# Performance work log

Measured on AMD Instinct MI355X. Metric: run time of the kernel, lower is better.

## Reference

```python
import jax, jax.numpy as jnp
import numpy as np

N_USERS = 40000
N_ITEMS = 20000
NNZ = 1_000_000
D = 64
N_LAYERS = 3
EPS = 1e-8
PRUNING = 0.0  # forward default: pruning=0.0 -> get_sim_adj branch, threshold is a no-op


def setup_inputs() -> dict:
    key = jax.random.key(0)
    k1, k2, k3 = jax.random.split(key, 3)
    # unique-ish sorted edge codes -> coalesced COO order (sorted by (u, i))
    codes = jnp.sort(jax.random.randint(k3, (NNZ,), 0, N_USERS * N_ITEMS, dtype=jnp.int32))
    u_idx = codes // N_ITEMS
    i_idx = codes % N_ITEMS
    # xavier_uniform bound = sqrt(6/(fan_in+fan_out))
    b_u = float(np.sqrt(6.0 / (N_ITEMS + D)))
    b_i = float(np.sqrt(6.0 / (N_USERS + D)))
    user_linear = jax.random.uniform(k1, (N_ITEMS, D), jnp.float32, -b_u, b_u)
    item_linear = jax.random.uniform(k2, (N_USERS, D), jnp.float32, -b_i, b_i)
    return {"user_linear": user_linear, "item_linear": item_linear,
            "u_idx": u_idx, "i_idx": i_idx}


def reference(user_linear, item_linear, u_idx, i_idx):
    seg = jax.ops.segment_sum
    N = N_USERS + N_ITEMS
    # get_all_user_embedding: inter @ user_linear  -> [n_users, D]
    user_emb = seg(user_linear[i_idx], u_idx, num_segments=N_USERS)
    # get_all_item_embedding: inter.T @ item_linear -> [n_items, D]
    item_emb = seg(item_linear[u_idx], i_idx, num_segments=N_ITEMS)

    # sp_cos_sim: per-edge cosine similarity (chunked loop in torch == one vectorized gather)
    u_n = user_emb / jnp.maximum(jnp.linalg.norm(user_emb, axis=1, keepdims=True), EPS)
    i_n = item_emb / jnp.maximum(jnp.linalg.norm(item_emb, axis=1, keepdims=True), EPS)
    sims = jnp.sum(u_n[u_idx] * i_n[i_idx], axis=1)  # [nnz]
    # torch builds the sim sparse tensor with requires_grad=False -> detached
    sims = jax.lax.stop_gradient(sims)

    # inter2adj: values = [sims sorted by (u,i); sims sorted by (i,u)]
    sim_value = (sims + 1.0) * 0.5
    sim_value = jnp.where(sim_value < PRUNING, 0.0, sim_value) if PRUNING > 0 else sim_value
    perm = jnp.argsort(i_idx.astype(jnp.int32) * N_USERS + u_idx)  # (i,u) coalesce order
    rows = jnp.concatenate([u_idx, i_idx[perm] + N_USERS])          # [2*nnz]
    cols = jnp.concatenate([i_idx + N_USERS, u_idx[perm]])
    vals = jnp.concatenate([sim_value, sim_value[perm]])

    # row-normalize: D^-1 * A  (get_sim_adj)
    diags = seg(vals, rows, num_segments=N) + 1e-7
    vals = vals * (1.0 / diags)[rows]

    # LightGCN-style propagation
    all_emb = jnp.concatenate([user_emb, item_emb], axis=0)  # [N, D]
    embs = [all_emb]
    for _ in range(N_LAYERS):
        all_emb = seg(all_emb[cols] * vals[:, None], rows, num_segments=N)
        embs.append(all_emb)
    out = jnp.mean(jnp.stack(embs, axis=1), axis=1)  # [N, D]
    return out[:N_USERS], out[N_USERS:]
```

## Files before the change

kernel.cpp:

```cpp
#include <hip/hip_runtime.h>
#include <hip/hip_fp16.h>

#define N_USERS 40000
#define N_ITEMS 20000
#define N_TOTAL (N_USERS + N_ITEMS)
#define D 64
#define G_BKT ((N_ITEMS + 63) >> 6)
#define PAD 16

union H8 { uint4 u; __half h[8]; };

#define ZA (N_ITEMS * D / 8)
#define ZB (N_USERS * D / 8)
#define ZC (N_USERS + 1)
#define ZD ((G_BKT + 1) * PAD)
#define ZTOT (ZA + ZB + ZC + ZD)

__global__ void setup_kernel(const float* __restrict__ ul, const float* __restrict__ il,
                             const int* __restrict__ u_idx,
                             __half* __restrict__ ulH, __half* __restrict__ ilH,
                             int* __restrict__ pu, int* __restrict__ bcnt, int nnz) {
    int t = blockIdx.x * blockDim.x + threadIdx.x;
    if (t < ZA) {
        const float4* s = (const float4*)(ul + (size_t)t * 8);
        float4 a = s[0], b = s[1];
        H8 o;
        o.h[0] = __float2half(a.x); o.h[1] = __float2half(a.y);
        o.h[2] = __float2half(a.z); o.h[3] = __float2half(a.w);
        o.h[4] = __float2half(b.x); o.h[5] = __float2half(b.y);
        o.h[6] = __float2half(b.z); o.h[7] = __float2half(b.w);
        ((uint4*)ulH)[t] = o.u;
    } else if (t < ZA + ZB) {
        int q = t - ZA;
        const float4* s = (const float4*)(il + (size_t)q * 8);
        float4 a = s[0], b = s[1];
        H8 o;
        o.h[0] = __float2half(a.x); o.h[1] = __float2half(a.y);
        o.h[2] = __float2half(a.z); o.h[3] = __float2half(a.w);
        o.h[4] = __float2half(b.x); o.h[5] = __float2half(b.y);
        o.h[6] = __float2half(b.z); o.h[7] = __float2half(b.w);
        ((uint4*)ilH)[q] = o.u;
    } else if (t < ZA + ZB + ZC) {
        int u = t - (ZA + ZB);
        int lo = 0, hi = nnz;
        while (lo < hi) { int mid = (lo + hi) >> 1; if (u_idx[mid] < u) lo = mid + 1; else hi = mid; }
        pu[u] = lo;
    } else if (t < ZTOT) {
        bcnt[t - (ZA + ZB + ZC)] = 0;
    }
}


__global__ void bcount_kernel(const int* __restrict__ i_idx, int* __restrict__ bcnt, int nnz) {
    __shared__ int lc[G_BKT];
    for (int t = threadIdx.x; t < G_BKT; t += blockDim.x) lc[t] = 0;
    __syncthreads();
    int stride = gridDim.x * blockDim.x;
    for (int e = blockIdx.x * blockDim.x + threadIdx.x; e < nnz; e += stride)
        atomicAdd(&lc[__builtin_nontemporal_load(i_idx + e) >> 6], 1);
    __syncthreads();
    for (int t = threadIdx.x; t < G_BKT; t += blockDim.x)
        if (lc[t]) atomicAdd(bcnt + t * PAD, lc[t]);
}

__global__ void bscan_kernel(const int* __restrict__ bcnt, int* __restrict__ bbase,
                             int* __restrict__ bcur, int* __restrict__ pi, int nnz) {
    if (threadIdx.x == 0 && blockIdx.x == 0) {
        int run = 0;
        for (int g = 0; g < G_BKT; ++g) {
            bbase[g * PAD] = run;
            bcur[g * PAD] = run;
            run += bcnt[g * PAD];
        }
        bbase[G_BKT * PAD] = run;
        pi[N_ITEMS] = run;
    }
}

__global__ void p1_kernel(const int* __restrict__ i_idx, const int* __restrict__ u_idx,
                          int* __restrict__ bcur, int2* __restrict__ tmp, int nnz) {
    const int E = 8;
    __shared__ int lc[G_BKT];
    __shared__ int gb[G_BKT];
    for (int t = threadIdx.x; t < G_BKT; t += blockDim.x) lc[t] = 0;
    __syncthreads();
    int base_e = blockIdx.x * blockDim.x * E;
    int myb[E], myr[E]; int2 myv[E];
    #pragma unroll
    for (int j = 0; j < E; ++j) {
        int e = base_e + j * blockDim.x + threadIdx.x;
        myb[j] = -1;
        if (e < nnz) {
            int i = __builtin_nontemporal_load(i_idx + e);
            int u = __builtin_nontemporal_load(u_idx + e);
            int b = i >> 6;
            myb[j] = b;
            myr[j] = atomicAdd(&lc[b], 1);
            myv[j] = make_int2(e, (i << 16) | u);
        }
    }
    __syncthreads();
    for (int t = threadIdx.x; t < G_BKT; t += blockDim.x)
        gb[t] = lc[t] ? atomicAdd(bcur + t * PAD, lc[t]) : 0;
    __syncthreads();
    #pragma unroll
    for (int j = 0; j < E; ++j)
        if (myb[j] >= 0) tmp[gb[myb[j]] + myr[j]] = myv[j];
}

__global__ void p2_kernel(const int2* __restrict__ tmp, const int* __restrict__ bbase,
                          int* __restrict__ pi, int* __restrict__ eids, int* __restrict__ col2) {
    __shared__ int hist[64];
    __shared__ int cur[64];
    int g = blockIdx.x;
    int t = threadIdx.x;
    if (t < 64) { hist[t] = 0; cur[t] = 0; }
    __syncthreads();
    int base = bbase[g * PAD], end = bbase[(g + 1) * PAD];
    int lo_item = g << 6;
    for (int k = base + t; k < end; k += blockDim.x)
        atomicAdd(&hist[(tmp[k].y >> 16) & 63], 1);
    __syncthreads();
    if (t == 0) {
        int run = base;
        for (int x = 0; x < 64; ++x) {
            int c = hist[x];
            hist[x] = run;
            if (lo_item + x < N_ITEMS) pi[lo_item + x] = run;
            run += c;
        }
    }
    __syncthreads();
    for (int k = base + t; k < end; k += blockDim.x) {
        int2 v = tmp[k];
        int li = (v.y >> 16) & 63;
        int pos = atomicAdd(&cur[li], 1);
        int dst = hist[li] + pos;
        eids[dst] = v.x;
        col2[dst] = v.y & 0xFFFF;
    }
}

__global__ void emb_kernel(const __half* __restrict__ ulH, const __half* __restrict__ ilH,
                           const int* __restrict__ i_idx, const int* __restrict__ col2,
                           const int* __restrict__ pu, const int* __restrict__ pi,
                           __half* __restrict__ embH, float* __restrict__ invn) {
    int tid = blockIdx.x * blockDim.x + threadIdx.x;
    int wave = tid >> 6, lane = threadIdx.x & 63;
    int g = lane >> 3, c = lane & 7;
    int row = wave * 8 + g;
    if (row >= N_TOTAL) return;
    float s[8];
    #pragma unroll
    for (int j = 0; j < 8; ++j) s[j] = 0.f;
    const __half* tbl; const int* cols; int b, e;
    if (row < N_USERS) { tbl = ulH; cols = i_idx; b = pu[row]; e = pu[row + 1]; }
    else { int i = row - N_USERS; tbl = ilH; cols = col2; b = pi[i]; e = pi[i + 1]; }
    int k = b;
    for (; k + 3 < e; k += 4) {
        int i0 = cols[k], i1 = cols[k + 1], i2 = cols[k + 2], i3 = cols[k + 3];
        H8 r0, r1, r2, r3;
        r0.u = ((const uint4*)(tbl + (size_t)i0 * D))[c];
        r1.u = ((const uint4*)(tbl + (size_t)i1 * D))[c];
        r2.u = ((const uint4*)(tbl + (size_t)i2 * D))[c];
        r3.u = ((const uint4*)(tbl + (size_t)i3 * D))[c];
        #pragma unroll
        for (int q = 0; q < 8; ++q)
            s[q] += (__half2float(r0.h[q]) + __half2float(r1.h[q]))
                  + (__half2float(r2.h[q]) + __half2float(r3.h[q]));
    }
    for (; k < e; ++k) {
        H8 r0;
        r0.u = ((const uint4*)(tbl + (size_t)cols[k] * D))[c];
        #pragma unroll
        for (int q = 0; q < 8; ++q) s[q] += __half2float(r0.h[q]);
    }
    float nsq = 0.f;
    #pragma unroll
    for (int q = 0; q < 8; ++q) nsq += s[q] * s[q];
    #pragma unroll
    for (int m = 1; m < 8; m <<= 1) nsq += __shfl_xor(nsq, m, 64);
    H8 o;
    #pragma unroll
    for (int q = 0; q < 8; ++q) o.h[q] = __float2half(s[q]);
    ((uint4*)(embH + (size_t)row * D))[c] = o.u;
    if (c == 0) invn[row] = 1.f / fmaxf(sqrtf(nsq), 1e-8f);
}

__global__ void fsp1u_kernel(const __half* __restrict__ embA, const float* __restrict__ invn,
                             const int* __restrict__ i_idx, const int* __restrict__ pu,
                             float* __restrict__ sims, float* __restrict__ diag,
                             __half* __restrict__ embB) {
    int tid = blockIdx.x * blockDim.x + threadIdx.x;
    int wave = tid >> 6, lane = threadIdx.x & 63;
    int g = lane >> 3, c = lane & 7;
    int u = wave * 8 + g;
    if (u >= N_USERS) return;
    float invu = invn[u];
    H8 ur; ur.u = ((const uint4*)(embA + (size_t)u * D))[c];
    float un[8];
    #pragma unroll
    for (int q = 0; q < 8; ++q) un[q] = __half2float(ur.h[q]) * invu;
    float s[8];
    #pragma unroll
    for (int q = 0; q < 8; ++q) s[q] = 0.f;
    float dsum = 0.f;
    int b = pu[u], e = pu[u + 1];
    int k = b;
    for (; k + 3 < e; k += 4) {
        int i0 = i_idx[k], i1 = i_idx[k + 1], i2 = i_idx[k + 2], i3 = i_idx[k + 3];
        H8 r0, r1, r2, r3;
        r0.u = ((const uint4*)(embA + (size_t)(N_USERS + i0) * D))[c];
        r1.u = ((const uint4*)(embA + (size_t)(N_USERS + i1) * D))[c];
        r2.u = ((const uint4*)(embA + (size_t)(N_USERS + i2) * D))[c];
        r3.u = ((const uint4*)(embA + (size_t)(N_USERS + i3) * D))[c];
        float iv0 = invn[N_USERS + i0], iv1 = invn[N_USERS + i1];
        float iv2 = invn[N_USERS + i2], iv3 = invn[N_USERS + i3];
        float d0 = 0.f, d1 = 0.f, d2 = 0.f, d3 = 0.f;
        #pragma unroll
        for (int q = 0; q < 8; ++q) {
            d0 += un[q] * __half2float(r0.h[q]);
            d1 += un[q] * __half2float(r1.h[q]);
            d2 += un[q] * __half2float(r2.h[q]);
            d3 += un[q] * __half2float(r3.h[q]);
        }
        #pragma unroll
        for (int m = 1; m < 8; m <<= 1) {
            d0 += __shfl_xor(d0, m, 64); d1 += __shfl_xor(d1, m, 64);
            d2 += __shfl_xor(d2, m, 64); d3 += __shfl_xor(d3, m, 64);
        }
        float sv0 = (d0 * iv0 + 1.f) * 0.5f;
        float sv1 = (d1 * iv1 + 1.f) * 0.5f;
        float sv2 = (d2 * iv2 + 1.f) * 0.5f;
        float sv3 = (d3 * iv3 + 1.f) * 0.5f;
        if (c == 0) { sims[k] = sv0; sims[k + 1] = sv1; sims[k + 2] = sv2; sims[k + 3] = sv3; }
        dsum += (sv0 + sv1) + (sv2 + sv3);
        #pragma unroll
        for (int q = 0; q < 8; ++q)
            s[q] += (sv0 * __half2float(r0.h[q]) + sv1 * __half2float(r1.h[q]))
                  + (sv2 * __half2float(r2.h[q]) + sv3 * __half2float(r3.h[q]));
    }
    for (; k < e; ++k) {
        int i0 = i_idx[k];
        H8 r0;
        r0.u = ((const uint4*)(embA + (size_t)(N_USERS + i0) * D))[c];
        float iv0 = invn[N_USERS + i0];
        float d0 = 0.f;
        #pragma unroll
        for (int q = 0; q < 8; ++q) d0 += un[q] * __half2float(r0.h[q]);
        #pragma unroll
        for (int m = 1; m < 8; m <<= 1) d0 += __shfl_xor(d0, m, 64);
        float sv0 = (d0 * iv0 + 1.f) * 0.5f;
        if (c == 0) sims[k] = sv0;
        dsum += sv0;
        #pragma unroll
        for (int q = 0; q < 8; ++q) s[q] += sv0 * __half2float(r0.h[q]);
    }
    if (c == 0) diag[u] = dsum;
    float invd = 1.f / (dsum + 1e-7f);
    H8 o;
    #pragma unroll
    for (int q = 0; q < 8; ++q) o.h[q] = __float2half(s[q] * invd);
    ((uint4*)(embB + (size_t)u * D))[c] = o.u;
}

__global__ void p1i_kernel(const __half* __restrict__ embA, const float* __restrict__ sims,
                           const int* __restrict__ eids, const int* __restrict__ col2,
                           const int* __restrict__ pi, float* __restrict__ w2,
                           float* __restrict__ diag, __half* __restrict__ embB) {
    int tid = blockIdx.x * blockDim.x + threadIdx.x;
    int wave = tid >> 6, lane = threadIdx.x & 63;
    int g = lane >> 3, c = lane & 7;
    int i = wave * 8 + g;
    if (i >= N_ITEMS) return;
    float s[8];
    #pragma unroll
    for (int q = 0; q < 8; ++q) s[q] = 0.f;
    float dsum = 0.f;
    int b = pi[i], e = pi[i + 1];
    int k = b;
    for (; k + 3 < e; k += 4) {
        int e0 = eids[k], e1 = eids[k + 1], e2 = eids[k + 2], e3 = eids[k + 3];
        int u0 = col2[k], u1 = col2[k + 1], u2 = col2[k + 2], u3 = col2[k + 3];
        float w0 = sims[e0], w1 = sims[e1], w2v = sims[e2], w3v = sims[e3];
        H8 r0, r1, r2, r3;
        r0.u = ((const uint4*)(embA + (size_t)u0 * D))[c];
        r1.u = ((const uint4*)(embA + (size_t)u1 * D))[c];
        r2.u = ((const uint4*)(embA + (size_t)u2 * D))[c];
        r3.u = ((const uint4*)(embA + (size_t)u3 * D))[c];
        if (c == 0) { w2[k] = w0; w2[k + 1] = w1; w2[k + 2] = w2v; w2[k + 3] = w3v; }
        dsum += (w0 + w1) + (w2v + w3v);
        #pragma unroll
        for (int q = 0; q < 8; ++q)
            s[q] += (w0 * __half2float(r0.h[q]) + w1 * __half2float(r1.h[q]))
                  + (w2v * __half2float(r2.h[q]) + w3v * __half2float(r3.h[q]));
    }
    for (; k < e; ++k) {
        float w0 = sims[eids[k]];
        H8 r0;
        r0.u = ((const uint4*)(embA + (size_t)col2[k] * D))[c];
        if (c == 0) w2[k] = w0;
        dsum += w0;
        #pragma unroll
        for (int q = 0; q < 8; ++q) s[q] += w0 * __half2float(r0.h[q]);
    }
    if (c == 0) diag[N_USERS + i] = dsum;
    float invd = 1.f / (dsum + 1e-7f);
    H8 o;
    #pragma unroll
    for (int q = 0; q < 8; ++q) o.h[q] = __float2half(s[q] * invd);
    ((uint4*)(embB + (size_t)(N_USERS + i) * D))[c] = o.u;
}

template <bool FINAL>
__global__ void prop_kernel(const __half* __restrict__ curH, __half* __restrict__ nextH,
                            const float* __restrict__ sims, const float* __restrict__ w2,
                            const float* __restrict__ diag,
                            const int* __restrict__ i_idx, const int* __restrict__ col2,
                            const int* __restrict__ pu, const int* __restrict__ pi,
                            const __half* __restrict__ e0, const __half* __restrict__ e1,
                            const __half* __restrict__ e2, float* __restrict__ out) {
    int tid = blockIdx.x * blockDim.x + threadIdx.x;
    int wave = tid >> 6, lane = threadIdx.x & 63;
    int g = lane >> 3, c = lane & 7;
    int row = wave * 8 + g;
    if (row >= N_TOTAL) return;
    float s[8];
    #pragma unroll
    for (int j = 0; j < 8; ++j) s[j] = 0.f;
    const int* cols; const float* ws; int b, e, colOff;
    if (row < N_USERS) { b = pu[row]; e = pu[row + 1]; cols = i_idx; ws = sims; colOff = N_USERS; }
    else { int i = row - N_USERS; b = pi[i]; e = pi[i + 1]; cols = col2; ws = w2; colOff = 0; }
    int k = b;
    for (; k + 3 < e; k += 4) {
        int i0 = cols[k] + colOff, i1 = cols[k + 1] + colOff,
            i2 = cols[k + 2] + colOff, i3 = cols[k + 3] + colOff;
        float w0 = ws[k], w1 = ws[k + 1], w2v = ws[k + 2], w3v = ws[k + 3];
        H8 r0, r1, r2, r3;
        r0.u = ((const uint4*)(curH + (size_t)i0 * D))[c];
        r1.u = ((const uint4*)(curH + (size_t)i1 * D))[c];
        r2.u = ((const uint4*)(curH + (size_t)i2 * D))[c];
        r3.u = ((const uint4*)(curH + (size_t)i3 * D))[c];
        #pragma unroll
        for (int q = 0; q < 8; ++q)
            s[q] += (w0 * __half2float(r0.h[q]) + w1 * __half2float(r1.h[q]))
                  + (w2v * __half2float(r2.h[q]) + w3v * __half2float(r3.h[q]));
    }
    for (; k < e; ++k) {
        float w0 = ws[k];
        H8 r0;
        r0.u = ((const uint4*)(curH + (size_t)(cols[k] + colOff) * D))[c];
        #pragma unroll
        for (int q = 0; q < 8; ++q) s[q] += w0 * __half2float(r0.h[q]);
    }
    float invd = 1.f / (diag[row] + 1e-7f);
    float v[8];
    #pragma unroll
    for (int q = 0; q < 8; ++q) v[q] = s[q] * invd;
    if (FINAL) {
        H8 r0, r1, r2;
        r0.u = ((const uint4*)(e0 + (size_t)row * D))[c];
        r1.u = ((const uint4*)(e1 + (size_t)row * D))[c];
        r2.u = ((const uint4*)(e2 + (size_t)row * D))[c];
        float o[8];
        #pragma unroll
        for (int q = 0; q < 8; ++q)
            o[q] = (v[q] + __half2float(r0.h[q]) + __half2float(r1.h[q]) + __half2float(r2.h[q])) * 0.25f;
        float4* op = (float4*)(out + (size_t)row * D);
        op[c * 2]     = make_float4(o[0], o[1], o[2], o[3]);
        op[c * 2 + 1] = make_float4(o[4], o[5], o[6], o[7]);
    } else {
        H8 o;
        #pragma unroll
        for (int q = 0; q < 8; ++q) o.h[q] = __float2half(v[q]);
        ((uint4*)(nextH + (size_t)row * D))[c] = o.u;
    }
}


extern "C" void kernel_launch(void* const* d_in, const int* in_sizes, int n_in,
                              void* d_out, int out_size, void* d_ws, size_t ws_size,
                              hipStream_t stream) {
    const float* user_linear = (const float*)d_in[0];
    const float* item_linear = (const float*)d_in[1];
    const int* u_idx = (const int*)d_in[2];
    const int* i_idx = (const int*)d_in[3];
    const int nnz = in_sizes[2];

    char* p = (char*)d_ws;
    auto carve = [&](size_t bytes) { void* r = (void*)p; p += (bytes + 255) & ~(size_t)255; return r; };
    __half* embA = (__half*)carve((size_t)N_TOTAL * D * 2);
    __half* embB = (__half*)carve((size_t)N_TOTAL * D * 2);
    __half* embC = (__half*)carve((size_t)N_TOTAL * D * 2);
    __half* ulH  = (__half*)carve((size_t)N_ITEMS * D * 2);
    __half* ilH  = (__half*)carve((size_t)N_USERS * D * 2);
    float* sims = (float*)carve((size_t)nnz * 4);
    float* w2   = (float*)carve((size_t)nnz * 4);
    float* diag = (float*)carve((size_t)N_TOTAL * 4);
    float* invn = (float*)carve((size_t)N_TOTAL * 4);
    int* pu   = (int*)carve((size_t)(N_USERS + 1) * 4);
    int* pi   = (int*)carve((size_t)(N_ITEMS + 1) * 4);
    int* eids = (int*)carve((size_t)nnz * 4);
    int* col2 = (int*)carve((size_t)nnz * 4);
    int* bcnt  = (int*)carve((size_t)(G_BKT + 1) * PAD * 4);
    int* bbase = (int*)carve((size_t)(G_BKT + 1) * PAD * 4);
    int* bcur  = (int*)carve((size_t)(G_BKT + 1) * PAD * 4);

    int2* tmp = (int2*)embA;

    float* out = (float*)d_out;

    const int B = 256;

    setup_kernel<<<(ZTOT + B - 1) / B, B, 0, stream>>>(user_linear, item_linear, u_idx,
                                                       ulH, ilH, pu, bcnt, nnz);
    bcount_kernel<<<256, B, 0, stream>>>(i_idx, bcnt, nnz);
    bscan_kernel<<<1, 64, 0, stream>>>(bcnt, bbase, bcur, pi, nnz);
    p1_kernel<<<(nnz + B * 8 - 1) / (B * 8), B, 0, stream>>>(i_idx, u_idx, bcur, tmp, nnz);
    p2_kernel<<<G_BKT, B, 0, stream>>>(tmp, bbase, pi, eids, col2);

    int rowThreads = ((N_TOTAL + 7) / 8) * 64;
    emb_kernel<<<(rowThreads + B - 1) / B, B, 0, stream>>>(ulH, ilH, i_idx, col2,
                                                           pu, pi, embA, invn);

    int uThreads = ((N_USERS + 7) / 8) * 64;
    fsp1u_kernel<<<(uThreads + B - 1) / B, B, 0, stream>>>(embA, invn, i_idx, pu,
                                                           sims, diag, embB);
    int iThreads = ((N_ITEMS + 7) / 8) * 64;
    p1i_kernel<<<(iThreads + B - 1) / B, B, 0, stream>>>(embA, sims, eids, col2, pi,
                                                         w2, diag, embB);

    prop_kernel<false><<<(rowThreads + B - 1) / B, B, 0, stream>>>(embB, embC, sims, w2, diag,
                                                                   i_idx, col2, pu, pi,
                                                                   nullptr, nullptr, nullptr, nullptr);
    prop_kernel<true><<<(rowThreads + B - 1) / B, B, 0, stream>>>(embC, nullptr, sims, w2, diag,
                                                                  i_idx, col2, pu, pi,
                                                                  embA, embB, embC, out);
}
```

Before: 232.8 us.

## Use nontemporal loads/stores for streamed data and remap row blocks across XCDs

Marks streamed index arrays, edge weights and per-row output writes as nontemporal so they do not evict the gathered embedding tables from cache. Also adds a block-to-row mapping for the full-grid kernels that interleaves blocks mod 8, so each XCD works on a contiguous range of user or item rows and the gathered rows stay local to that XCD's L2. The gain depends on hardware cache behaviour. The hardcoded grid mapping ties the code to the fixed problem sizes.

Result: slower. 336.6 us (+44.6%).

```diff
diff --git a/kernel.cpp b/kernel.cpp
--- a/kernel.cpp
+++ b/kernel.cpp
@@ -9,6 +9,40 @@
 #define PAD 16
 
 union H8 { uint4 u; __half h[8]; };
+
+typedef unsigned int u32x4 __attribute__((ext_vector_type(4)));
+typedef float f32x4 __attribute__((ext_vector_type(4)));
+typedef int i32x2 __attribute__((ext_vector_type(2)));
+
+#define NTL(x) __builtin_nontemporal_load(&(x))
+
+__device__ __forceinline__ void nt_store_u4(uint4 v, void* p) {
+    u32x4 t = { v.x, v.y, v.z, v.w };
+    __builtin_nontemporal_store(t, (u32x4*)p);
+}
+__device__ __forceinline__ void nt_store_f4(float4 v, void* p) {
+    f32x4 t = { v.x, v.y, v.z, v.w };
+    __builtin_nontemporal_store(t, (f32x4*)p);
+}
+__device__ __forceinline__ int2 nt_load_i2(const void* p) {
+    i32x2 t = __builtin_nontemporal_load((const i32x2*)p);
+    return make_int2(t.x, t.y);
+}
+
+__device__ __forceinline__ int map_row(int bid, int wib, int g) {
+    int x = bid & 7, s = bid >> 3;
+    if (x < 5) {
+        int ub = x * 250 + s;
+        if (ub >= 1250) return -1;
+        return ub * 32 + wib * 8 + g;
+    } else {
+        int si = x - 5;
+        int cnt = (si == 2) ? 207 : 209;
+        if (s >= cnt) return -1;
+        return N_USERS + (si * 209 + s) * 32 + wib * 8 + g;
+    }
+}
+#define GRID_FULL 2000
 
 #define ZA (N_ITEMS * D / 8)
 #define ZB (N_USERS * D / 8)
@@ -119,7 +153,7 @@
     int base = bbase[g * PAD], end = bbase[(g + 1) * PAD];
     int lo_item = g << 6;
     for (int k = base + t; k < end; k += blockDim.x)
-        atomicAdd(&hist[(tmp[k].y >> 16) & 63], 1);
+        atomicAdd(&hist[(nt_load_i2(&tmp[k]).y >> 16) & 63], 1);
     __syncthreads();
     if (t == 0) {
         int run = base;
@@ -132,7 +166,7 @@
     }
     __syncthreads();
     for (int k = base + t; k < end; k += blockDim.x) {
-        int2 v = tmp[k];
+        int2 v = nt_load_i2(&tmp[k]);
         int li = (v.y >> 16) & 63;
         int pos = atomicAdd(&cur[li], 1);
         int dst = hist[li] + pos;
@@ -145,11 +179,10 @@
                            const int* __restrict__ i_idx, const int* __restrict__ col2,
                            const int* __restrict__ pu, const int* __restrict__ pi,
                            __half* __restrict__ embH, float* __restrict__ invn) {
-    int tid = blockIdx.x * blockDim.x + threadIdx.x;
-    int wave = tid >> 6, lane = threadIdx.x & 63;
+    int wib = threadIdx.x >> 6, lane = threadIdx.x & 63;
     int g = lane >> 3, c = lane & 7;
-    int row = wave * 8 + g;
-    if (row >= N_TOTAL) return;
+    int row = map_row(blockIdx.x, wib, g);
+    if (row < 0) return;
     float s[8];
     #pragma unroll
     for (int j = 0; j < 8; ++j) s[j] = 0.f;
@@ -158,7 +191,7 @@
     else { int i = row - N_USERS; tbl = ilH; cols = col2; b = pi[i]; e = pi[i + 1]; }
     int k = b;
     for (; k + 3 < e; k += 4) {
-        int i0 = cols[k], i1 = cols[k + 1], i2 = cols[k + 2], i3 = cols[k + 3];
+        int i0 = NTL(cols[k]), i1 = NTL(cols[k + 1]), i2 = NTL(cols[k + 2]), i3 = NTL(cols[k + 3]);
         H8 r0, r1, r2, r3;
         r0.u = ((const uint4*)(tbl + (size_t)i0 * D))[c];
         r1.u = ((const uint4*)(tbl + (size_t)i1 * D))[c];
@@ -171,7 +204,7 @@
     }
     for (; k < e; ++k) {
         H8 r0;
-        r0.u = ((const uint4*)(tbl + (size_t)cols[k] * D))[c];
+        r0.u = ((const uint4*)(tbl + (size_t)NTL(cols[k]) * D))[c];
         #pragma unroll
         for (int q = 0; q < 8; ++q) s[q] += __half2float(r0.h[q]);
     }
@@ -183,7 +216,7 @@
     H8 o;
     #pragma unroll
     for (int q = 0; q < 8; ++q) o.h[q] = __float2half(s[q]);
-    ((uint4*)(embH + (size_t)row * D))[c] = o.u;
+    nt_store_u4(o.u, (uint4*)(embH + (size_t)row * D) + c);
     if (c == 0) invn[row] = 1.f / fmaxf(sqrtf(nsq), 1e-8f);
 }
 
@@ -208,7 +241,7 @@
     int b = pu[u], e = pu[u + 1];
     int k = b;
     for (; k + 3 < e; k += 4) {
-        int i0 = i_idx[k], i1 = i_idx[k + 1], i2 = i_idx[k + 2], i3 = i_idx[k + 3];
+        int i0 = NTL(i_idx[k]), i1 = NTL(i_idx[k + 1]), i2 = NTL(i_idx[k + 2]), i3 = NTL(i_idx[k + 3]);
         H8 r0, r1, r2, r3;
         r0.u = ((const uint4*)(embA + (size_t)(N_USERS + i0) * D))[c];
         r1.u = ((const uint4*)(embA + (size_t)(N_USERS + i1) * D))[c];
@@ -233,7 +266,12 @@
         float sv1 = (d1 * iv1 + 1.f) * 0.5f;
         float sv2 = (d2 * iv2 + 1.f) * 0.5f;
         float sv3 = (d3 * iv3 + 1.f) * 0.5f;
-        if (c == 0) { sims[k] = sv0; sims[k + 1] = sv1; sims[k + 2] = sv2; sims[k + 3] = sv3; }
+        if (c == 0) {
+            __builtin_nontemporal_store(sv0, sims + k);
+            __builtin_nontemporal_store(sv1, sims + k + 1);
+            __builtin_nontemporal_store(sv2, sims + k + 2);
+            __builtin_nontemporal_store(sv3, sims + k + 3);
+        }
         dsum += (sv0 + sv1) + (sv2 + sv3);
         #pragma unroll
         for (int q = 0; q < 8; ++q)
@@ -241,7 +279,7 @@
                   + (sv2 * __half2float(r2.h[q]) + sv3 * __half2float(r3.h[q]));
     }
     for (; k < e; ++k) {
-        int i0 = i_idx[k];
+        int i0 = NTL(i_idx[k]);
         H8 r0;
         r0.u = ((const uint4*)(embA + (size_t)(N_USERS + i0) * D))[c];
         float iv0 = invn[N_USERS + i0];
@@ -251,7 +289,7 @@
         #pragma unroll
         for (int m = 1; m < 8; m <<= 1) d0 += __shfl_xor(d0, m, 64);
         float sv0 = (d0 * iv0 + 1.f) * 0.5f;
-        if (c == 0) sims[k] = sv0;
+        if (c == 0) __builtin_nontemporal_store(sv0, sims + k);
         dsum += sv0;
         #pragma unroll
         for (int q = 0; q < 8; ++q) s[q] += sv0 * __half2float(r0.h[q]);
@@ -261,7 +299,7 @@
     H8 o;
     #pragma unroll
     for (int q = 0; q < 8; ++q) o.h[q] = __float2half(s[q] * invd);
-    ((uint4*)(embB + (size_t)u * D))[c] = o.u;
+    nt_store_u4(o.u, (uint4*)(embB + (size_t)u * D) + c);
 }
 
 __global__ void p1i_kernel(const __half* __restrict__ embA, const float* __restrict__ sims,
@@ -280,15 +318,20 @@
     int b = pi[i], e = pi[i + 1];
     int k = b;
     for (; k + 3 < e; k += 4) {
-        int e0 = eids[k], e1 = eids[k + 1], e2 = eids[k + 2], e3 = eids[k + 3];
-        int u0 = col2[k], u1 = col2[k + 1], u2 = col2[k + 2], u3 = col2[k + 3];
+        int e0 = NTL(eids[k]), e1 = NTL(eids[k + 1]), e2 = NTL(eids[k + 2]), e3 = NTL(eids[k + 3]);
+        int u0 = NTL(col2[k]), u1 = NTL(col2[k + 1]), u2 = NTL(col2[k + 2]), u3 = NTL(col2[k + 3]);
         float w0 = sims[e0], w1 = sims[e1], w2v = sims[e2], w3v = sims[e3];
         H8 r0, r1, r2, r3;
         r0.u = ((const uint4*)(embA + (size_t)u0 * D))[c];
         r1.u = ((const uint4*)(embA + (size_t)u1 * D))[c];
         r2.u = ((const uint4*)(embA + (size_t)u2 * D))[c];
         r3.u = ((const uint4*)(embA + (size_t)u3 * D))[c];
-        if (c == 0) { w2[k] = w0; w2[k + 1] = w1; w2[k + 2] = w2v; w2[k + 3] = w3v; }
+        if (c == 0) {
+            __builtin_nontemporal_store(w0, w2 + k);
+            __builtin_nontemporal_store(w1, w2 + k + 1);
+            __builtin_nontemporal_store(w2v, w2 + k + 2);
+            __builtin_nontemporal_store(w3v, w2 + k + 3);
+        }
         dsum += (w0 + w1) + (w2v + w3v);
         #pragma unroll
         for (int q = 0; q < 8; ++q)
@@ -296,10 +339,10 @@
                   + (w2v * __half2float(r2.h[q]) + w3v * __half2float(r3.h[q]));
     }
     for (; k < e; ++k) {
-        float w0 = sims[eids[k]];
+        float w0 = sims[NTL(eids[k])];
         H8 r0;
-        r0.u = ((const uint4*)(embA + (size_t)col2[k] * D))[c];
-        if (c == 0) w2[k] = w0;
+        r0.u = ((const uint4*)(embA + (size_t)NTL(col2[k]) * D))[c];
+        if (c == 0) __builtin_nontemporal_store(w0, w2 + k);
         dsum += w0;
         #pragma unroll
         for (int q = 0; q < 8; ++q) s[q] += w0 * __half2float(r0.h[q]);
@@ -309,7 +352,7 @@
     H8 o;
     #pragma unroll
     for (int q = 0; q < 8; ++q) o.h[q] = __float2half(s[q] * invd);
-    ((uint4*)(embB + (size_t)(N_USERS + i) * D))[c] = o.u;
+    nt_store_u4(o.u, (uint4*)(embB + (size_t)(N_USERS + i) * D) + c);
 }
 
 template <bool FINAL>
@@ -320,11 +363,10 @@
                             const int* __restrict__ pu, const int* __restrict__ pi,
                             const __half* __restrict__ e0, const __half* __restrict__ e1,
                             const __half* __restrict__ e2, float* __restrict__ out) {
-    int tid = blockIdx.x * blockDim.x + threadIdx.x;
-    int wave = tid >> 6, lane = threadIdx.x & 63;
+    int wib = threadIdx.x >> 6, lane = threadIdx.x & 63;
     int g = lane >> 3, c = lane & 7;
-    int row = wave * 8 + g;
-    if (row >= N_TOTAL) return;
+    int row = map_row(blockIdx.x, wib, g);
+    if (row < 0) return;
     float s[8];
     #pragma unroll
     for (int j = 0; j < 8; ++j) s[j] = 0.f;
@@ -333,9 +375,9 @@
     else { int i = row - N_USERS; b = pi[i]; e = pi[i + 1]; cols = col2; ws = w2; colOff = 0; }
     int k = b;
     for (; k + 3 < e; k += 4) {
-        int i0 = cols[k] + colOff, i1 = cols[k + 1] + colOff,
-            i2 = cols[k + 2] + colOff, i3 = cols[k + 3] + colOff;
-        float w0 = ws[k], w1 = ws[k + 1], w2v = ws[k + 2], w3v = ws[k + 3];
+        int i0 = NTL(cols[k]) + colOff, i1 = NTL(cols[k + 1]) + colOff,
+            i2 = NTL(cols[k + 2]) + colOff, i3 = NTL(cols[k + 3]) + colOff;
+        float w0 = NTL(ws[k]), w1 = NTL(ws[k + 1]), w2v = NTL(ws[k + 2]), w3v = NTL(ws[k + 3]);
         H8 r0, r1, r2, r3;
         r0.u = ((const uint4*)(curH + (size_t)i0 * D))[c];
         r1.u = ((const uint4*)(curH + (size_t)i1 * D))[c];
@@ -347,9 +389,9 @@
                   + (w2v * __half2float(r2.h[q]) + w3v * __half2float(r3.h[q]));
     }
     for (; k < e; ++k) {
-        float w0 = ws[k];
+        float w0 = NTL(ws[k]);
         H8 r0;
-        r0.u = ((const uint4*)(curH + (size_t)(cols[k] + colOff) * D))[c];
+        r0.u = ((const uint4*)(curH + (size_t)(NTL(cols[k]) + colOff) * D))[c];
         #pragma unroll
         for (int q = 0; q < 8; ++q) s[q] += w0 * __half2float(r0.h[q]);
     }
@@ -359,21 +401,24 @@
     for (int q = 0; q < 8; ++q) v[q] = s[q] * invd;
     if (FINAL) {
         H8 r0, r1, r2;
-        r0.u = ((const uint4*)(e0 + (size_t)row * D))[c];
-        r1.u = ((const uint4*)(e1 + (size_t)row * D))[c];
-        r2.u = ((const uint4*)(e2 + (size_t)row * D))[c];
+        u32x4 t0 = __builtin_nontemporal_load((const u32x4*)(e0 + (size_t)row * D) + c);
+        u32x4 t1 = __builtin_nontemporal_load((const u32x4*)(e1 + (size_t)row * D) + c);
+        u32x4 t2 = __builtin_nontemporal_load((const u32x4*)(e2 + (size_t)row * D) + c);
+        r0.u = make_uint4(t0.x, t0.y, t0.z, t0.w);
+        r1.u = make_uint4(t1.x, t1.y, t1.z, t1.w);
+        r2.u = make_uint4(t2.x, t2.y, t2.z, t2.w);
         float o[8];
         #pragma unroll
         for (int q = 0; q < 8; ++q)
             o[q] = (v[q] + __half2float(r0.h[q]) + __half2float(r1.h[q]) + __half2float(r2.h[q])) * 0.25f;
         float4* op = (float4*)(out + (size_t)row * D);
-        op[c * 2]     = make_float4(o[0], o[1], o[2], o[3]);
-        op[c * 2 + 1] = make_float4(o[4], o[5], o[6], o[7]);
+        nt_store_f4(make_float4(o[0], o[1], o[2], o[3]), op + c * 2);
+        nt_store_f4(make_float4(o[4], o[5], o[6], o[7]), op + c * 2 + 1);
     } else {
         H8 o;
         #pragma unroll
         for (int q = 0; q < 8; ++q) o.h[q] = __float2half(v[q]);
-        ((uint4*)(nextH + (size_t)row * D))[c] = o.u;
+        nt_store_u4(o.u, (uint4*)(nextH + (size_t)row * D) + c);
     }
 }
 
@@ -419,9 +464,7 @@
     p1_kernel<<<(nnz + B * 8 - 1) / (B * 8), B, 0, stream>>>(i_idx, u_idx, bcur, tmp, nnz);
     p2_kernel<<<G_BKT, B, 0, stream>>>(tmp, bbase, pi, eids, col2);
 
-    int rowThreads = ((N_TOTAL + 7) / 8) * 64;
-    emb_kernel<<<(rowThreads + B - 1) / B, B, 0, stream>>>(ulH, ilH, i_idx, col2,
-                                                           pu, pi, embA, invn);
+    emb_kernel<<<GRID_FULL, B, 0, stream>>>(ulH, ilH, i_idx, col2, pu, pi, embA, invn);
 
     int uThreads = ((N_USERS + 7) / 8) * 64;
     fsp1u_kernel<<<(uThreads + B - 1) / B, B, 0, stream>>>(embA, invn, i_idx, pu,
@@ -430,10 +473,10 @@
     p1i_kernel<<<(iThreads + B - 1) / B, B, 0, stream>>>(embA, sims, eids, col2, pi,
                                                          w2, diag, embB);
 
-    prop_kernel<false><<<(rowThreads + B - 1) / B, B, 0, stream>>>(embB, embC, sims, w2, diag,
-                                                                   i_idx, col2, pu, pi,
-                                                                   nullptr, nullptr, nullptr, nullptr);
-    prop_kernel<true><<<(rowThreads + B - 1) / B, B, 0, stream>>>(embC, nullptr, sims, w2, diag,
-                                                                  i_idx, col2, pu, pi,
-                                                                  embA, embB, embC, out);
-}
+    prop_kernel<false><<<GRID_FULL, B, 0, stream>>>(embB, embC, sims, w2, diag,
+                                                    i_idx, col2, pu, pi,
+                                                    nullptr, nullptr, nullptr, nullptr);
+    prop_kernel<true><<<GRID_FULL, B, 0, stream>>>(embC, nullptr, sims, w2, diag,
+                                                   i_idx, col2, pu, pi,
+                                                   embA, embB, embC, out);
+}
```
